# Performance work log

Measured on AMD Instinct MI355X. Metric: run time of the kernel, lower is better.

The kernel has to match this reference:

```python
import jax, jax.numpy as jnp
import numpy as np

B, S, D = 4, 2048, 1024
NEG = -1e10

def setup_inputs() -> dict:
    key = jax.random.key(0)
    ks = jax.random.split(key, 10)
    inv = 1.0 / np.sqrt(D)
    return {
        "Q": jax.random.normal(ks[0], (B, S, D), dtype=jnp.float32),
        "K": jax.random.normal(ks[1], (B, S, D), dtype=jnp.float32),
        "V": jax.random.normal(ks[2], (B, S, D), dtype=jnp.float32),
        "attention_mask": jax.random.randint(ks[3], (B, 1, S), 0, 2, dtype=jnp.int32),
        "Wq": jax.random.uniform(ks[4], (D, D), jnp.float32, -inv, inv),
        "bq": jnp.zeros((D,), jnp.float32),
        "Wk": jax.random.uniform(ks[5], (D, D), jnp.float32, -inv, inv),
        "bk": jnp.zeros((D,), jnp.float32),
        "Wv": jax.random.uniform(ks[6], (D, D), jnp.float32, -inv, inv),
        "bv": jnp.zeros((D,), jnp.float32),
    }

def reference(Q, K, V, attention_mask, Wq, bq, Wk, bk, Wv, bv):
    # QKV projections (dropout is identity in eval mode)
    q = jnp.einsum('bsd,ed->bse', Q, Wq) + bq  # [B,S,D]
    k = jnp.einsum('bsd,ed->bse', K, Wk) + bk
    v = jnp.einsum('bsd,ed->bse', V, Wv) + bv
    scores = jnp.einsum('bqd,bkd->bqk', q, k) / jnp.sqrt(jnp.float32(D))  # [B,S,S]
    scores = jnp.where(attention_mask == 0, jnp.float32(NEG), scores)
    # additive causal mask: upper triangle (diag=1) gets NEG
    causal = jnp.triu(jnp.full((S, S), NEG, dtype=jnp.float32), k=1)
    scores = scores + causal
    attn = jax.nn.softmax(scores, axis=-1)
    return jnp.einsum('bqk,bkd->bqd', attn, v)
```

## Files before the change

### kernel.cpp

```cpp
#include <hip/hip_runtime.h>
#include <hip/hip_bf16.h>

typedef __bf16 bf16x8 __attribute__((ext_vector_type(8)));
typedef float floatx4 __attribute__((ext_vector_type(4)));
typedef unsigned short ushort_t;

__device__ __forceinline__ bf16x8 load8f(const float* p) {
  const float4* q = reinterpret_cast<const float4*>(p);
  float4 x = q[0], y = q[1];
  bf16x8 r;
  r[0] = (__bf16)x.x; r[1] = (__bf16)x.y; r[2] = (__bf16)x.z; r[3] = (__bf16)x.w;
  r[4] = (__bf16)y.x; r[5] = (__bf16)y.y; r[6] = (__bf16)y.z; r[7] = (__bf16)y.w;
  return r;
}

__device__ __forceinline__ void storeC(float* C, long idx, float v) { C[idx] = v; }
__device__ __forceinline__ void storeC(ushort_t* C, long idx, float v) {
  __bf16 b = (__bf16)v;
  C[idx] = __builtin_bit_cast(ushort_t, b);
}

__device__ __forceinline__ void glds16(const ushort_t* g, ushort_t* l) {
  __builtin_amdgcn_global_load_lds(
      (const __attribute__((address_space(1))) void*)g,
      (__attribute__((address_space(3))) void*)l, 16, 0, 0);
}

__device__ __forceinline__ void bar_raw()  { asm volatile("s_barrier" ::: "memory"); }
__device__ __forceinline__ void lgkm0()    { asm volatile("s_waitcnt lgkmcnt(0)" ::: "memory"); }
__device__ __forceinline__ void wait_vm4() { asm volatile("s_waitcnt vmcnt(4)" ::: "memory"); }
__device__ __forceinline__ void wait_vm0() { asm volatile("s_waitcnt vmcnt(0)" ::: "memory"); }

__global__ __launch_bounds__(256) void cvt3(
    const float* __restrict__ s0, const float* __restrict__ s1,
    const float* __restrict__ s2, ushort_t* __restrict__ dst, long n,
    const int* __restrict__ mask, int* __restrict__ j0, int S, int B)
{
  const int z = blockIdx.y;
  const float* s = (z == 0) ? s0 : ((z == 1) ? s1 : s2);
  ushort_t* d = dst + (long)z * n;
  const long i = (((long)blockIdx.x * 256) + threadIdx.x) * 8;
  if (i < n) {
    bf16x8 v = load8f(s + i);
    *reinterpret_cast<bf16x8*>(d + i) = v;
  }
  if (mask && z == 0 && (int)blockIdx.x < B) {
    const int b = blockIdx.x;
    const int* m = mask + (long)b * S;
    const int tid = threadIdx.x;
    int best = S;
    for (int j = tid; j < S; j += 256)
      if (m[j] != 0) best = min(best, j);
    #pragma unroll
    for (int off = 32; off; off >>= 1)
      best = min(best, __shfl_xor(best, off));
    __shared__ int red[4];
    if ((tid & 63) == 0) red[tid >> 6] = best;
    __syncthreads();
    if (tid == 0) j0[b] = min(min(red[0], red[1]), min(red[2], red[3]));
  }
}

template<typename TC>
__device__ __forceinline__ void gemm256_core(
    const ushort_t* __restrict__ Apan,
    const ushort_t* __restrict__ Bpan,
    const float* __restrict__ bias, int bias_mode,
    TC* __restrict__ C, int bm, int bn, int N, int K, int G, float alpha)
{
  __shared__ ushort_t Ab[2][2][128 * 64];
  __shared__ ushort_t Bb[2][2][128 * 64];

  const int tid = threadIdx.x;
  const int wv = tid >> 6;
  const int lane = tid & 63;
  const int wr = wv >> 2, wc = wv & 3;
  const int lr = lane & 15, lq = lane >> 4;

  const int q0 = tid << 4;
  const int r0 = q0 >> 7;
  const int c0 = ((q0 & 127) ^ ((r0 & 7) << 4)) >> 1;
  const int lo0 = q0 >> 1;
  const int lo1 = lo0 + 4096;
  const long Kl = K;

  const ushort_t* As0 = Apan + (long)r0 * Kl + c0;
  const ushort_t* Bs0 = Bpan + (long)r0 * Kl + c0;

  auto stA = [&](int t, int h) {
    const ushort_t* s = As0 + (long)(h * 128) * Kl + t * 64;
    ushort_t* d = &Ab[t & 1][h][0];
    glds16(s, d + lo0);
    glds16(s + 64 * Kl, d + lo1);
  };
  auto stB = [&](int t, int h) {
    const ushort_t* s = Bs0 + (long)(h * 128) * Kl + t * 64;
    ushort_t* d = &Bb[t & 1][h][0];
    glds16(s, d + lo0);
    glds16(s + 64 * Kl, d + lo1);
  };

  const int aco0 = ((lq * 16) ^ ((lr & 7) << 4)) >> 1;
  const int aco1 = ((64 + lq * 16) ^ ((lr & 7) << 4)) >> 1;

  floatx4 acc[8][4];
  #pragma unroll
  for (int i = 0; i < 8; ++i)
    #pragma unroll
    for (int j = 0; j < 4; ++j)
      acc[i][j] = (floatx4){0.f, 0.f, 0.f, 0.f};

  bf16x8 a0[4][2], a1[4][2], b0[2][2], b1[2][2];

  auto ldA4 = [&](bf16x8 (&a)[4][2], int buf, int i0) {
    const ushort_t* Ah = &Ab[buf][wr][lr * 64];
    #pragma unroll
    for (int i = 0; i < 4; ++i) {
      a[i][0] = *reinterpret_cast<const bf16x8*>(Ah + (i0 + i) * 1024 + aco0);
      a[i][1] = *reinterpret_cast<const bf16x8*>(Ah + (i0 + i) * 1024 + aco1);
    }
  };
  auto ldB2 = [&](bf16x8 (&b)[2][2], int buf, int j0) {
    const ushort_t* Bh = &Bb[buf][wc >> 1][(wc & 1) * 4096 + lr * 64];
    #pragma unroll
    for (int j = 0; j < 2; ++j) {
      b[j][0] = *reinterpret_cast<const bf16x8*>(Bh + (j0 + j) * 1024 + aco0);
      b[j][1] = *reinterpret_cast<const bf16x8*>(Bh + (j0 + j) * 1024 + aco1);
    }
  };
  auto MM = [&](int I0, bf16x8 (&AF)[4][2], int J0, bf16x8 (&BF)[2][2]) {
    #pragma unroll
    for (int i = 0; i < 4; ++i)
      #pragma unroll
      for (int j = 0; j < 2; ++j) {
        acc[I0 + i][J0 + j] = __builtin_amdgcn_mfma_f32_16x16x32_bf16(
            AF[i][0], BF[j][0], acc[I0 + i][J0 + j], 0, 0, 0);
        acc[I0 + i][J0 + j] = __builtin_amdgcn_mfma_f32_16x16x32_bf16(
            AF[i][1], BF[j][1], acc[I0 + i][J0 + j], 0, 0, 0);
      }
  };

  stB(0, 0); stB(0, 1);
  stA(0, 0); stA(0, 1);
  stB(1, 0); stB(1, 1);
  wait_vm4();
  bar_raw();

  for (int t = 0; t < G; ++t) {
    const int buf = t & 1;
    ldA4(a0, buf, 0);
    ldB2(b0, buf, 0);
    if (t + 1 < G) stA(t + 1, 0);
    bar_raw(); lgkm0();
    __builtin_amdgcn_s_setprio(1);
    MM(0, a0, 0, b0);
    __builtin_amdgcn_s_setprio(0);
    bar_raw();
    ldB2(b1, buf, 2);
    if (t + 1 < G) stA(t + 1, 1);
    bar_raw(); lgkm0();
    __builtin_amdgcn_s_setprio(1);
    MM(0, a0, 2, b1);
    __builtin_amdgcn_s_setprio(0);
    bar_raw();
    ldA4(a1, buf, 4);
    if (t + 2 < G) stB(t + 2, 0);
    bar_raw(); lgkm0();
    __builtin_amdgcn_s_setprio(1);
    MM(4, a1, 0, b0);
    __builtin_amdgcn_s_setprio(0);
    bar_raw();
    if (t + 2 < G) { stB(t + 2, 1); wait_vm4(); }
    else if (t + 1 < G) wait_vm0();
    bar_raw(); lgkm0();
    __builtin_amdgcn_s_setprio(1);
    MM(4, a1, 2, b1);
    __builtin_amdgcn_s_setprio(0);
    bar_raw();
  }

  #pragma unroll
  for (int i = 0; i < 8; ++i) {
    #pragma unroll
    for (int j = 0; j < 4; ++j) {
      const int row0 = bm * 256 + wr * 128 + i * 16 + lq * 4;
      const int col  = bn * 256 + wc * 64 + j * 16 + lr;
      #pragma unroll
      for (int r = 0; r < 4; ++r) {
        float v = acc[i][j][r] * alpha;
        if (bias_mode == 1) v += bias[col];
        else if (bias_mode == 2) v += bias[row0 + r];
        storeC(C, (long)(row0 + r) * N + col, v);
      }
    }
  }
}

__global__ __launch_bounds__(512) void proj8(
    const ushort_t* __restrict__ Qb, const ushort_t* __restrict__ Wqb,
    const float* __restrict__ bq, const float* __restrict__ bk,
    const float* __restrict__ bv,
    ushort_t* __restrict__ qk, ushort_t* __restrict__ vT,
    long NQ, long NW)
{
  const int s = blockIdx.x;
  int bm, bn, N, mode;
  const ushort_t *A, *Bp;
  ushort_t* Cc;
  const float* bias;
  if (s < 256) {
    const int z = s >> 7, r = s & 127;
    bm = r >> 2; bn = r & 3;
    A  = Qb + (long)z * NQ + (long)bm * 256 * 1024;
    Bp = Wqb + (long)z * NW + (long)bn * 256 * 1024;
    Cc = qk + (long)z * NQ;
    bias = z ? bk : bq; mode = 1; N = 1024;
  } else {
    const int u = s - 256, vb = u >> 5, r = u & 31;
    bm = r >> 3; bn = r & 7;
    A  = Wqb + 2 * NW + (long)bm * 256 * 1024;
    Bp = Qb + 2 * NQ + (long)vb * (2048L * 1024) + (long)bn * 256 * 1024;
    Cc = vT + (long)vb * (1024L * 2048);
    bias = bv; mode = 2; N = 2048;
  }
  gemm256_core<ushort_t>(A, Bp, bias, mode, Cc, bm, bn, N, 1024, 16, 1.0f);
}

__global__ __launch_bounds__(512) void scores8(
    const ushort_t* __restrict__ qb, const ushort_t* __restrict__ kb,
    ushort_t* __restrict__ Sc, const int* __restrict__ j0p)
{
  const int bz = blockIdx.z;
  const int s = blockIdx.x + (blockIdx.y << 3);
  int bm, bn;
  if (s < 36) {
    int r = 0;
    while ((r + 1) * (r + 2) / 2 <= s) ++r;
    bm = r; bn = s - r * (r + 1) / 2;
  } else {
    int u = s - 36, r = 0;
    while (u >= 7 - r) { u -= 7 - r; ++r; }
    bm = r; bn = r + 1 + u;
  }
  if (bn > bm && j0p[bz] <= bm * 256) return;
  const long SD = 2048L * 1024;
  gemm256_core<ushort_t>(qb + (long)bz * SD + (long)bm * 256 * 1024,
                         kb + (long)bz * SD + (long)bn * 256 * 1024,
                         nullptr, 0, Sc + (long)bz * 2048 * 2048,
                         bm, bn, 2048, 1024, 16, 0.03125f);
}

__global__ __launch_bounds__(512) void pv8(
    const ushort_t* __restrict__ P, const ushort_t* __restrict__ vT,
    float* __restrict__ out, const int* __restrict__ j0p)
{
  const int bz = blockIdx.z;
  const int bm = 7 - blockIdx.x;
  const int bn = blockIdx.y;
  int G = 32;
  if (j0p[bz] <= bm * 256) G = (bm + 1) * 4;
  gemm256_core<float>(P + (long)bz * 2048 * 2048 + (long)bm * 256 * 2048,
                      vT + (long)bz * 1024 * 2048 + (long)bn * 256 * 2048,
                      nullptr, 0, out + (long)bz * 2048 * 1024,
                      bm, bn, 1024, 2048, G, 1.0f);
}

__global__ __launch_bounds__(256) void softmax_causal(
    const ushort_t* __restrict__ Sc, ushort_t* __restrict__ P,
    const int* __restrict__ mask, const int* __restrict__ j0p, int S)
{
  const int i = blockIdx.x, b = blockIdx.y;
  const ushort_t* row = Sc + ((long)b * S + i) * S;
  ushort_t* prow = P + ((long)b * S + i) * S;
  const int* mrow = mask + (long)b * S;
  const int tid = threadIdx.x;
  const int lane = tid & 63, wave = tid >> 6;
  const int j0 = tid * 8;
  __shared__ float red[4];

  const int blk = i >> 8;
  const int jmax = (j0p[b] <= (blk << 8)) ? ((blk + 1) << 8) : S;
  const bool act = (j0 < jmax);

  float vals[8];
  float mymax = -3.4e38f;
  if (act) {
    bf16x8 sv = *reinterpret_cast<const bf16x8*>(row + j0);
    const int4* mp = reinterpret_cast<const int4*>(mrow + j0);
    int4 m0 = mp[0], m1 = mp[1];
    int mk[8] = {m0.x, m0.y, m0.z, m0.w, m1.x, m1.y, m1.z, m1.w};
    #pragma unroll
    for (int u = 0; u < 8; ++u) {
      const int j = j0 + u;
      float v = (float)sv[u];
      if (mk[u] == 0) v = -1e10f;
      if (j > i) v += -1e10f;
      vals[u] = v;
      mymax = fmaxf(mymax, v);
    }
  }
  #pragma unroll
  for (int off = 32; off; off >>= 1)
    mymax = fmaxf(mymax, __shfl_xor(mymax, off));
  if (lane == 0) red[wave] = mymax;
  __syncthreads();
  const float m = fmaxf(fmaxf(red[0], red[1]), fmaxf(red[2], red[3]));
  __syncthreads();

  float sum = 0.f;
  if (act) {
    #pragma unroll
    for (int u = 0; u < 8; ++u) {
      const float e = __expf(vals[u] - m);
      vals[u] = e;
      sum += e;
    }
  }
  #pragma unroll
  for (int off = 32; off; off >>= 1)
    sum += __shfl_xor(sum, off);
  if (lane == 0) red[wave] = sum;
  __syncthreads();
  const float tot = red[0] + red[1] + red[2] + red[3];
  const float inv = 1.0f / tot;

  if (act) {
    bf16x8 pv;
    #pragma unroll
    for (int u = 0; u < 8; ++u) pv[u] = (__bf16)(vals[u] * inv);
    *reinterpret_cast<bf16x8*>(prow + j0) = pv;
  }
}

extern "C" void kernel_launch(void* const* d_in, const int* in_sizes, int n_in,
                              void* d_out, int out_size, void* d_ws, size_t ws_size,
                              hipStream_t stream)
{
  const int B = 4, S = 2048, D = 1024;
  const float* Q  = (const float*)d_in[0];
  const float* K  = (const float*)d_in[1];
  const float* V  = (const float*)d_in[2];
  const int*   am = (const int*)d_in[3];
  const float* Wq = (const float*)d_in[4];
  const float* bq = (const float*)d_in[5];
  const float* Wk = (const float*)d_in[6];
  const float* bk = (const float*)d_in[7];
  const float* Wv = (const float*)d_in[8];
  const float* bv = (const float*)d_in[9];
  float* out = (float*)d_out;

  const long MS = (long)B * S;
  const long NQ = MS * D;
  const long NW = (long)D * D;

  ushort_t* qb = (ushort_t*)d_ws;
  ushort_t* kb = qb + NQ;
  ushort_t* vT = kb + NQ;
  ushort_t* Qb = vT + NQ;
  ushort_t* Wqb = Qb + 3 * NQ;
  int* j0 = (int*)(Wqb + 3 * NW);
  ushort_t* Sc = Qb;
  ushort_t* P  = qb;

  cvt3<<<dim3((int)(NQ / 2048), 3), dim3(256), 0, stream>>>(Q, K, V, Qb, NQ, am, j0, S, B);
  cvt3<<<dim3((int)(NW / 2048), 3), dim3(256), 0, stream>>>(Wq, Wk, Wv, Wqb, NW,
                                                            nullptr, nullptr, S, B);

  proj8<<<dim3(384), dim3(512), 0, stream>>>(Qb, Wqb, bq, bk, bv, qb, vT, NQ, NW);

  scores8<<<dim3(8, 8, 4), dim3(512), 0, stream>>>(qb, kb, Sc, j0);

  softmax_causal<<<dim3(S, B), dim3(256), 0, stream>>>(Sc, P, am, j0, S);

  pv8<<<dim3(8, 4, 4), dim3(512), 0, stream>>>(P, vT, out, j0);
}
```

Baseline: 341.8 us.

## Split-K the PV GEMM, merge conversion launches, remap block ids across XCDs

Merges the activation and weight fp32-to-bf16 conversions into one launch. Remaps block indices in proj8, scores8 and pv8 so that consecutive blocks go to different XCDs in strided groups. Splits the PV GEMM along K into two halves for rows with large K extent, writing the second half into a scratch buffer that a new combine kernel adds to the output. This raises PV parallelism from 128 to up to 256 blocks and balances the causal workload, at the cost of an extra output-sized read/write pass and one more launch.

```diff
diff --git a/kernel.cpp b/kernel.cpp
--- a/kernel.cpp
+++ b/kernel.cpp
@@ -31,20 +31,32 @@
 __device__ __forceinline__ void wait_vm4() { asm volatile("s_waitcnt vmcnt(4)" ::: "memory"); }
 __device__ __forceinline__ void wait_vm0() { asm volatile("s_waitcnt vmcnt(0)" ::: "memory"); }
 
-__global__ __launch_bounds__(256) void cvt3(
-    const float* __restrict__ s0, const float* __restrict__ s1,
-    const float* __restrict__ s2, ushort_t* __restrict__ dst, long n,
+__global__ __launch_bounds__(256) void cvt3m(
+    const float* __restrict__ Q, const float* __restrict__ K,
+    const float* __restrict__ V, const float* __restrict__ Wq,
+    const float* __restrict__ Wk, const float* __restrict__ Wv,
+    ushort_t* __restrict__ dstQ, ushort_t* __restrict__ dstW,
+    long nq, long nw,
     const int* __restrict__ mask, int* __restrict__ j0, int S, int B)
 {
   const int z = blockIdx.y;
-  const float* s = (z == 0) ? s0 : ((z == 1) ? s1 : s2);
-  ushort_t* d = dst + (long)z * n;
-  const long i = (((long)blockIdx.x * 256) + threadIdx.x) * 8;
+  const long bq = nq >> 11;
+  long x = blockIdx.x;
+  const float* s; ushort_t* d; long n;
+  if (x < bq) {
+    s = (z == 0) ? Q : ((z == 1) ? K : V);
+    d = dstQ + (long)z * nq; n = nq;
+  } else {
+    x -= bq;
+    s = (z == 0) ? Wq : ((z == 1) ? Wk : Wv);
+    d = dstW + (long)z * nw; n = nw;
+  }
+  const long i = ((x * 256) + threadIdx.x) * 8;
   if (i < n) {
     bf16x8 v = load8f(s + i);
     *reinterpret_cast<bf16x8*>(d + i) = v;
   }
-  if (mask && z == 0 && (int)blockIdx.x < B) {
+  if (z == 0 && (int)blockIdx.x < B) {
     const int b = blockIdx.x;
     const int* m = mask + (long)b * S;
     const int tid = threadIdx.x;
@@ -203,7 +215,8 @@
     ushort_t* __restrict__ qk, ushort_t* __restrict__ vT,
     long NQ, long NW)
 {
-  const int s = blockIdx.x;
+  const int h = blockIdx.x;
+  const int s = (h & 7) * 48 + (h >> 3);
   int bm, bn, N, mode;
   const ushort_t *A, *Bp;
   ushort_t* Cc;
@@ -230,8 +243,10 @@
     const ushort_t* __restrict__ qb, const ushort_t* __restrict__ kb,
     ushort_t* __restrict__ Sc, const int* __restrict__ j0p)
 {
-  const int bz = blockIdx.z;
-  const int s = blockIdx.x + (blockIdx.y << 3);
+  const int h = blockIdx.x;
+  const int job = (h & 7) * 32 + (h >> 3);
+  const int bz = job >> 6;
+  const int s = job & 63;
   int bm, bn;
   if (s < 36) {
     int r = 0;
@@ -252,17 +267,53 @@
 
 __global__ __launch_bounds__(512) void pv8(
     const ushort_t* __restrict__ P, const ushort_t* __restrict__ vT,
-    float* __restrict__ out, const int* __restrict__ j0p)
-{
-  const int bz = blockIdx.z;
-  const int bm = 7 - blockIdx.x;
-  const int bn = blockIdx.y;
-  int G = 32;
-  if (j0p[bz] <= bm * 256) G = (bm + 1) * 4;
-  gemm256_core<float>(P + (long)bz * 2048 * 2048 + (long)bm * 256 * 2048,
-                      vT + (long)bz * 1024 * 2048 + (long)bn * 256 * 2048,
-                      nullptr, 0, out + (long)bz * 2048 * 1024,
-                      bm, bn, 1024, 2048, G, 1.0f);
+    float* __restrict__ out, float* __restrict__ scr,
+    const int* __restrict__ j0p)
+{
+  const int h = blockIdx.x;
+  const int job = (h & 7) * 32 + (h >> 3);
+  const int bz = job >> 6;
+  const int r = job & 63;
+  const int bm = r >> 3;
+  const int kh = (r >> 2) & 1;
+  const int bn = r & 3;
+
+  const int Gf = (j0p[bz] <= bm * 256) ? (bm + 1) * 4 : 32;
+  int g0, g1;
+  if (Gf > 8) {
+    const int half = Gf >> 1;
+    g0 = kh ? half : 0;
+    g1 = kh ? Gf : half;
+  } else {
+    if (kh) return;
+    g0 = 0; g1 = Gf;
+  }
+
+  float* Cc = kh ? (scr + (long)bz * (2048L * 1024))
+                 : (out + (long)bz * (2048L * 1024));
+  gemm256_core<float>(
+      P  + (long)bz * (2048L * 2048) + (long)bm * 256 * 2048 + g0 * 64,
+      vT + (long)bz * (1024L * 2048) + (long)bn * 256 * 2048 + g0 * 64,
+      nullptr, 0, Cc, bm, bn, 1024, 2048, g1 - g0, 1.0f);
+}
+
+__global__ __launch_bounds__(256) void pv_combine(
+    float* __restrict__ out, const float* __restrict__ scr,
+    const int* __restrict__ j0p)
+{
+  const long u = (((long)blockIdx.x * 256) + threadIdx.x) * 8;
+  const int bz = (int)(u >> 21);
+  const long rem = u & ((1L << 21) - 1);
+  const int row = (int)(rem >> 10);
+  const int bm = row >> 8;
+  const int Gf = (j0p[bz] <= bm * 256) ? (bm + 1) * 4 : 32;
+  if (Gf <= 8) return;
+  float4* o = reinterpret_cast<float4*>(out + u);
+  const float4* s = reinterpret_cast<const float4*>(scr + u);
+  float4 o0 = o[0], o1 = o[1], s0 = s[0], s1 = s[1];
+  o0.x += s0.x; o0.y += s0.y; o0.z += s0.z; o0.w += s0.w;
+  o1.x += s1.x; o1.y += s1.y; o1.z += s1.z; o1.w += s1.w;
+  o[0] = o0; o[1] = o1;
 }
 
 __global__ __launch_bounds__(256) void softmax_causal(
@@ -361,16 +412,17 @@
   int* j0 = (int*)(Wqb + 3 * NW);
   ushort_t* Sc = Qb;
   ushort_t* P  = qb;
-
-  cvt3<<<dim3((int)(NQ / 2048), 3), dim3(256), 0, stream>>>(Q, K, V, Qb, NQ, am, j0, S, B);
-  cvt3<<<dim3((int)(NW / 2048), 3), dim3(256), 0, stream>>>(Wq, Wk, Wv, Wqb, NW,
-                                                            nullptr, nullptr, S, B);
+  float* scr   = (float*)Qb;
+
+  cvt3m<<<dim3((int)(NQ / 2048 + NW / 2048), 3), dim3(256), 0, stream>>>(
+      Q, K, V, Wq, Wk, Wv, Qb, Wqb, NQ, NW, am, j0, S, B);
 
   proj8<<<dim3(384), dim3(512), 0, stream>>>(Qb, Wqb, bq, bk, bv, qb, vT, NQ, NW);
 
-  scores8<<<dim3(8, 8, 4), dim3(512), 0, stream>>>(qb, kb, Sc, j0);
+  scores8<<<dim3(256), dim3(512), 0, stream>>>(qb, kb, Sc, j0);
 
   softmax_causal<<<dim3(S, B), dim3(256), 0, stream>>>(Sc, P, am, j0, S);
 
-  pv8<<<dim3(8, 4, 4), dim3(512), 0, stream>>>(P, vT, out, j0);
-}
+  pv8<<<dim3(256), dim3(512), 0, stream>>>(P, vT, out, scr, j0);
+  pv_combine<<<dim3((int)(MS * D / 8 / 256)), dim3(256), 0, stream>>>(out, scr, j0);
+}
```

New measurement: 322.5 us. 5.6% less time.
